# Kernel tuning notes

Hardware: AMD Instinct MI355X
Metric: run time of the kernel (lower is better)

Reference implementation:

```python
import jax, jax.numpy as jnp
import numpy as np

B, L, D = 1, 512, 128
DI = D // 2  # intermediate_dim = pair_dim // 2
EPS = 1e-5


def setup_inputs() -> dict:
    key = jax.random.key(0)
    ks = jax.random.split(key, 8)
    s = 0.02
    return {
        "pair": jax.random.normal(ks[0], (B, L, L, D), dtype=jnp.float32),
        "mask": jnp.ones((B, L, L), dtype=jnp.float32),
        "Wg1": jax.random.normal(ks[1], (D, DI), dtype=jnp.float32) * s,
        "bg1": jnp.zeros((DI,), dtype=jnp.float32),
        "Wg2": jax.random.normal(ks[2], (D, DI), dtype=jnp.float32) * s,
        "bg2": jnp.zeros((DI,), dtype=jnp.float32),
        "Wp": jax.random.normal(ks[3], (DI, D), dtype=jnp.float32) * s,
        "bp": jnp.zeros((D,), dtype=jnp.float32),
        "gamma": jnp.ones((D,), dtype=jnp.float32),
        "beta": jnp.zeros((D,), dtype=jnp.float32),
    }


def reference(pair, mask, Wg1, bg1, Wg2, bg2, Wp, bp, gamma, beta):
    # dual linear projections: [B,L,L,D] -> [B,L,L,DI]
    g1 = pair @ Wg1 + bg1
    g2 = pair @ Wg2 + bg2
    # outgoing triangle contraction: per-channel LxL matmul over k
    p = jnp.einsum("bikd,bkjd->bijd", g1, g2)  # [B,L,L,DI]
    p = p * mask[..., None]
    p = p @ Wp + bp  # [B,L,L,D]
    # dropout is identity in eval mode
    x = pair + p
    mu = jnp.mean(x, axis=-1, keepdims=True)
    var = jnp.var(x, axis=-1, keepdims=True)
    return (x - mu) * jax.lax.rsqrt(var + EPS) * gamma + beta
```

## Files before the change

kernel.cpp:

```cpp
#include <hip/hip_runtime.h>

#define L 512
#define LL (512*512)
#define D 128
#define DI 64

typedef unsigned short u16;
typedef short bf8 __attribute__((ext_vector_type(8)));
typedef float f4 __attribute__((ext_vector_type(4)));

union B8 { bf8 v; u16 u[8]; uint4 q; };

__device__ inline u16 f2bf(float f) {
  unsigned u = __builtin_bit_cast(unsigned, f);
  unsigned r = (u + 0x7FFFu + ((u >> 16) & 1u)) >> 16;
  return (u16)r;
}

__global__ __launch_bounds__(512)
void k1(const float* __restrict__ pair, const float* __restrict__ Wg1,
        const float* __restrict__ bg1, const float* __restrict__ Wg2,
        const float* __restrict__ bg2, u16* __restrict__ g1t, u16* __restrict__ g2t)
{
  __shared__ u16 WL[128*128];
  __shared__ u16 OL[64*256];
  const int tid = threadIdx.x;
  const int w = tid >> 6, lane = tid & 63;
  const int llo = lane & 15, lhi = lane >> 4;
  const int bx = blockIdx.x;
  const int i0 = (bx >> 5) << 4;
  const int c0 = (bx & 31) << 4;

  {
    const int n = tid >> 2;
    const int kb = (tid & 3) << 5;
    const float* src = (n < 64) ? (Wg1 + n) : (Wg2 + (n - 64));
    const int xr = (n & 7) << 3;
    for (int q = 0; q < 32; ++q) {
      int k = kb + q;
      WL[n*128 + (k ^ xr)] = f2bf(src[(size_t)k * 64]);
    }
  }
  __syncthreads();

  f4 acc[2][8];
  #pragma unroll
  for (int a = 0; a < 2; ++a)
    #pragma unroll
    for (int b = 0; b < 8; ++b) acc[a][b] = (f4){0.f,0.f,0.f,0.f};

  #pragma unroll
  for (int ks = 0; ks < 4; ++ks) {
    B8 bfr[8];
    const int kel = ks*32 + lhi*8;
    #pragma unroll
    for (int nf = 0; nf < 8; ++nf) {
      int n = nf*16 + llo;
      bfr[nf].q = *(const uint4*)&WL[n*128 + (kel ^ ((n & 7) << 3))];
    }
    #pragma unroll
    for (int mf = 0; mf < 2; ++mf) {
      int r = w*2 + mf;
      const float* ap = pair + (size_t)((i0 + r)*L + c0 + llo)*D + kel;
      float4 a0 = *(const float4*)ap;
      float4 a1 = *(const float4*)(ap + 4);
      B8 av;
      av.u[0]=f2bf(a0.x); av.u[1]=f2bf(a0.y); av.u[2]=f2bf(a0.z); av.u[3]=f2bf(a0.w);
      av.u[4]=f2bf(a1.x); av.u[5]=f2bf(a1.y); av.u[6]=f2bf(a1.z); av.u[7]=f2bf(a1.w);
      #pragma unroll
      for (int nf = 0; nf < 8; ++nf)
        acc[mf][nf] = __builtin_amdgcn_mfma_f32_16x16x32_bf16(av.v, bfr[nf].v, acc[mf][nf], 0, 0, 0);
    }
  }

  float bias[8];
  #pragma unroll
  for (int nf = 0; nf < 8; ++nf) {
    int n = nf*16 + llo;
    bias[nf] = (n < 64) ? bg1[n] : bg2[n - 64];
  }

  #pragma unroll
  for (int h = 0; h < 2; ++h) {
    __syncthreads();
    #pragma unroll
    for (int nf4 = 0; nf4 < 4; ++nf4) {
      const int nf = h*4 + nf4;
      const int chl = nf*16 + llo - h*64;
      const int xr = (chl & 7) << 2;
      #pragma unroll
      for (int mf = 0; mf < 2; ++mf) {
        const int r = w*2 + mf;
        const int cb = lhi*4;
        union { u16 h4[4]; uint2 d2; } vb;
        #pragma unroll
        for (int e = 0; e < 4; ++e) vb.h4[e] = f2bf(acc[mf][nf][e] + bias[nf]);
        if (h == 0) {
          int p = (r*16 + cb) ^ xr;
          *(uint2*)&OL[chl*256 + p] = vb.d2;
        } else {
          #pragma unroll
          for (int e = 0; e < 4; ++e)
            OL[chl*256 + (((cb + e)*16 + r) ^ xr)] = vb.h4[e];
        }
      }
    }
    __syncthreads();
    u16* dst0 = (h == 0) ? g1t : g2t;
    #pragma unroll
    for (int t2 = 0; t2 < 2; ++t2) {
      const int q = tid*2 + t2;
      const int chl = q >> 4;
      const int li = q & 15;
      const int xr = (chl & 7) << 2;
      union { u16 h4[16]; uint4 q4[2]; uint2 d2[4]; } tb;
      #pragma unroll
      for (int s = 0; s < 4; ++s) {
        int p = (li*16 + s*4) ^ xr;
        tb.d2[s] = *(const uint2*)&OL[chl*256 + p];
      }
      size_t off = (h == 0)
        ? ((size_t)chl*LL + (size_t)(i0 + li)*L + (size_t)c0)
        : ((size_t)chl*LL + (size_t)(c0 + li)*L + (size_t)i0);
      *(uint4*)(dst0 + off)     = tb.q4[0];
      *(uint4*)(dst0 + off + 8) = tb.q4[1];
    }
  }
}

__global__ __launch_bounds__(256)
void k2(const u16* __restrict__ g1t, const u16* __restrict__ g2t, u16* __restrict__ pt)
{
  __shared__ u16 SM[128*128];
  const int tid = threadIdx.x;
  const int lane = tid & 63, w = tid >> 6;
  const int llo = lane & 15, lhi = lane >> 4;
  const int bx = blockIdx.x;
  const int wg = ((bx & 7) << 7) | (bx >> 3);
  const int d  = wg >> 4;
  const int i0 = ((wg >> 2) & 3) << 7;
  const int j0 = (wg & 3) << 7;

  const u16* Ag = g1t + (size_t)d*LL;
  const u16* Yg = g2t + (size_t)d*LL;

  f4 acc[4][4];
  #pragma unroll
  for (int a = 0; a < 4; ++a)
    #pragma unroll
    for (int b = 0; b < 4; ++b) acc[a][b] = (f4){0.f,0.f,0.f,0.f};

  const int wr = (w >> 1) * 64, wc = (w & 1) * 64;

  const int srow = tid & 127;
  const u16* sg = (tid < 128) ? (Ag + (size_t)(i0 + srow)*L) : (Yg + (size_t)(j0 + srow)*L);
  u16* sl = (tid < 128) ? SM : (SM + 8192);
  const int sx = (srow & 7) << 3;

  for (int kt = 0; kt < 8; ++kt) {
    const int k0 = kt*64;
    #pragma unroll
    for (int q = 0; q < 8; ++q) {
      uint4 vv = *(const uint4*)(sg + k0 + q*8);
      *(uint4*)&sl[srow*64 + ((q*8) ^ sx)] = vv;
    }
    __syncthreads();
    #pragma unroll
    for (int ks = 0; ks < 2; ++ks) {
      B8 af[4], yf[4];
      const int kel = ks*32 + lhi*8;
      #pragma unroll
      for (int f = 0; f < 4; ++f) {
        int ra = wr + f*16 + llo;
        af[f].q = *(const uint4*)&SM[ra*64 + (kel ^ ((ra & 7) << 3))];
        int ry = wc + f*16 + llo;
        yf[f].q = *(const uint4*)&SM[8192 + ry*64 + (kel ^ ((ry & 7) << 3))];
      }
      #pragma unroll
      for (int mf = 0; mf < 4; ++mf)
        #pragma unroll
        for (int nf = 0; nf < 4; ++nf)
          acc[mf][nf] = __builtin_amdgcn_mfma_f32_16x16x32_bf16(af[mf].v, yf[nf].v, acc[mf][nf], 0, 0, 0);
    }
    __syncthreads();
  }

  #pragma unroll
  for (int mf = 0; mf < 4; ++mf) {
    #pragma unroll
    for (int nf = 0; nf < 4; ++nf) {
      const int jj = wc + nf*16 + llo;
      #pragma unroll
      for (int e = 0; e < 4; ++e) {
        const int ii = wr + mf*16 + lhi*4 + e;
        SM[ii*128 + (jj ^ ((ii & 7) << 3))] = f2bf(acc[mf][nf][e]);
      }
    }
  }
  __syncthreads();
  {
    const int ii = tid >> 1;
    const int half = (tid & 1) << 6;
    u16* dst = pt + (size_t)d*LL + (size_t)(i0 + ii)*L + j0 + half;
    const int xr = (ii & 7) << 3;
    #pragma unroll
    for (int q = 0; q < 8; ++q)
      *(uint4*)(dst + q*8) = *(const uint4*)&SM[ii*128 + ((half + q*8) ^ xr)];
  }
}

__global__ __launch_bounds__(256)
void k3(const u16* __restrict__ pt, const float* __restrict__ pair,
        const float* __restrict__ mask, const float* __restrict__ Wp,
        const float* __restrict__ bp, const float* __restrict__ gamma,
        const float* __restrict__ beta, float* __restrict__ out)
{
  __shared__ u16 PL[128*64];
  __shared__ u16 WT[128*64];
  __shared__ float MS[128];
  const int tid = threadIdx.x;
  const int lane = tid & 63, w = tid >> 6;
  const int llo = lane & 15, lhi = lane >> 4;
  const int bx = blockIdx.x;
  const int i  = bx >> 2;
  const int j0 = (bx & 3) << 7;

  {
    const int n = tid >> 1;
    const int dh = (tid & 1) << 5;
    const int xr = (n & 7) << 3;
    for (int q = 0; q < 32; ++q) {
      int dd = dh + q;
      WT[n*64 + (dd ^ xr)] = f2bf(Wp[(size_t)dd*128 + n]);
    }
  }
  if (tid < 128) MS[tid] = mask[(size_t)i*L + j0 + tid];
  {
    const int dd = tid >> 2;
    const u16* src = pt + (size_t)dd*LL + (size_t)i*L + j0;
    #pragma unroll
    for (int c = 0; c < 4; ++c) {
      const int jl = ((tid & 3)*4 + c) * 8;
      uint4 vv = *(const uint4*)(src + jl);
      const u16* pv = (const u16*)&vv;
      #pragma unroll
      for (int e = 0; e < 8; ++e) {
        int p = jl + e;
        PL[p*64 + (dd ^ ((p & 7) << 3))] = pv[e];
      }
    }
  }
  __syncthreads();

  f4 acc[2][8];
  #pragma unroll
  for (int a = 0; a < 2; ++a)
    #pragma unroll
    for (int b = 0; b < 8; ++b) acc[a][b] = (f4){0.f,0.f,0.f,0.f};

  #pragma unroll
  for (int ks = 0; ks < 2; ++ks) {
    const int kel = ks*32 + lhi*8;
    B8 bf[8];
    #pragma unroll
    for (int nf = 0; nf < 8; ++nf) {
      int n = nf*16 + llo;
      bf[nf].q = *(const uint4*)&WT[n*64 + (kel ^ ((n & 7) << 3))];
    }
    #pragma unroll
    for (int mf = 0; mf < 2; ++mf) {
      int p = w*32 + mf*16 + llo;
      B8 av;
      av.q = *(const uint4*)&PL[p*64 + (kel ^ ((p & 7) << 3))];
      #pragma unroll
      for (int nf = 0; nf < 8; ++nf)
        acc[mf][nf] = __builtin_amdgcn_mfma_f32_16x16x32_bf16(av.v, bf[nf].v, acc[mf][nf], 0, 0, 0);
    }
  }

  float bpv[8], gv[8], bv[8];
  #pragma unroll
  for (int nf = 0; nf < 8; ++nf) {
    int n = nf*16 + llo;
    bpv[nf] = bp[n]; gv[nf] = gamma[n]; bv[nf] = beta[n];
  }

  const size_t rowbase = (size_t)i*L + j0;
  #pragma unroll
  for (int mf = 0; mf < 2; ++mf) {
    #pragma unroll
    for (int e = 0; e < 4; ++e) {
      const int pl = w*32 + mf*16 + lhi*4 + e;
      const float mk = MS[pl];
      const float* prow = pair + (rowbase + pl)*D;
      float xv[8];
      float s1 = 0.f, s2 = 0.f;
      #pragma unroll
      for (int nf = 0; nf < 8; ++nf) {
        int n = nf*16 + llo;
        float x = prow[n] + mk*acc[mf][nf][e] + bpv[nf];
        xv[nf] = x; s1 += x; s2 += x*x;
      }
      #pragma unroll
      for (int m = 1; m < 16; m <<= 1) {
        s1 += __shfl_xor(s1, m);
        s2 += __shfl_xor(s2, m);
      }
      const float mu = s1 * (1.0f/128.0f);
      const float var = s2 * (1.0f/128.0f) - mu*mu;
      const float rs = rsqrtf(var + 1e-5f);
      float* orow = out + (rowbase + pl)*D;
      #pragma unroll
      for (int nf = 0; nf < 8; ++nf) {
        int n = nf*16 + llo;
        orow[n] = (xv[nf] - mu)*rs*gv[nf] + bv[nf];
      }
    }
  }
}

extern "C" void kernel_launch(void* const* d_in, const int* in_sizes, int n_in,
                              void* d_out, int out_size, void* d_ws, size_t ws_size,
                              hipStream_t stream) {
  (void)in_sizes; (void)n_in; (void)out_size; (void)ws_size;
  const float* pair = (const float*)d_in[0];
  const float* mask = (const float*)d_in[1];
  const float* Wg1  = (const float*)d_in[2];
  const float* bg1  = (const float*)d_in[3];
  const float* Wg2  = (const float*)d_in[4];
  const float* bg2  = (const float*)d_in[5];
  const float* Wp   = (const float*)d_in[6];
  const float* bp   = (const float*)d_in[7];
  const float* gamma= (const float*)d_in[8];
  const float* beta = (const float*)d_in[9];
  float* out = (float*)d_out;

  u16* g1t = (u16*)d_ws;
  u16* g2t = g1t + (size_t)DI*LL;
  u16* pt  = g2t + (size_t)DI*LL;

  hipLaunchKernelGGL(k1, dim3(1024), dim3(512), 0, stream,
                     pair, Wg1, bg1, Wg2, bg2, g1t, g2t);
  hipLaunchKernelGGL(k2, dim3(1024), dim3(256), 0, stream, g1t, g2t, pt);
  hipLaunchKernelGGL(k3, dim3(2048), dim3(256), 0, stream,
                     pt, pair, mask, Wp, bp, gamma, beta, out);
}
```

Baseline: 374.2 us.

## Pre-convert weights in a prep kernel, direct g1 stores, register-prefetch k2 tiles

```diff
diff --git a/kernel.cpp b/kernel.cpp
--- a/kernel.cpp
+++ b/kernel.cpp
@@ -17,13 +17,27 @@
   return (u16)r;
 }
 
+__global__ __launch_bounds__(256)
+void k0(const float* __restrict__ Wg1, const float* __restrict__ Wg2,
+        u16* __restrict__ WT)
+{
+  const int tid = threadIdx.x;
+  #pragma unroll
+  for (int it = 0; it < 4; ++it) {
+    const int E = blockIdx.x*1024 + it*256 + tid;
+    const int n = E >> 7, k = E & 127;
+    const float v = (n < 64) ? Wg1[(size_t)k*64 + n] : Wg2[(size_t)k*64 + (n - 64)];
+    WT[E] = f2bf(v);
+  }
+}
+
 __global__ __launch_bounds__(512)
-void k1(const float* __restrict__ pair, const float* __restrict__ Wg1,
-        const float* __restrict__ bg1, const float* __restrict__ Wg2,
-        const float* __restrict__ bg2, u16* __restrict__ g1t, u16* __restrict__ g2t)
+void k1(const float* __restrict__ pair, const u16* __restrict__ WT,
+        const float* __restrict__ bg1, const float* __restrict__ bg2,
+        u16* __restrict__ g1t, u16* __restrict__ g2t)
 {
   __shared__ u16 WL[128*128];
-  __shared__ u16 OL[64*256];
+  __shared__ u16 OL[32*256];
   const int tid = threadIdx.x;
   const int w = tid >> 6, lane = tid & 63;
   const int llo = lane & 15, lhi = lane >> 4;
@@ -31,15 +45,13 @@
   const int i0 = (bx >> 5) << 4;
   const int c0 = (bx & 31) << 4;
 
-  {
-    const int n = tid >> 2;
-    const int kb = (tid & 3) << 5;
-    const float* src = (n < 64) ? (Wg1 + n) : (Wg2 + (n - 64));
-    const int xr = (n & 7) << 3;
-    for (int q = 0; q < 32; ++q) {
-      int k = kb + q;
-      WL[n*128 + (k ^ xr)] = f2bf(src[(size_t)k * 64]);
-    }
+  #pragma unroll
+  for (int it = 0; it < 4; ++it) {
+    const int f = it*512 + tid;
+    const int E = f*8;
+    const int n = E >> 7, k = E & 127;
+    uint4 v = *(const uint4*)(WT + E);
+    *(uint4*)&WL[n*128 + (k ^ ((n & 7) << 3))] = v;
   }
   __syncthreads();
 
@@ -81,50 +93,48 @@
   }
 
   #pragma unroll
-  for (int h = 0; h < 2; ++h) {
-    __syncthreads();
-    #pragma unroll
-    for (int nf4 = 0; nf4 < 4; ++nf4) {
-      const int nf = h*4 + nf4;
-      const int chl = nf*16 + llo - h*64;
+  for (int nf = 0; nf < 4; ++nf) {
+    const int ch = nf*16 + llo;
+    #pragma unroll
+    for (int mf = 0; mf < 2; ++mf) {
+      const int r = w*2 + mf;
+      union { u16 h4[4]; uint2 d2; } vb;
+      #pragma unroll
+      for (int e = 0; e < 4; ++e) vb.h4[e] = f2bf(acc[mf][nf][e] + bias[nf]);
+      *(uint2*)(g1t + (size_t)ch*LL + (size_t)(i0 + r)*L + c0 + lhi*4) = vb.d2;
+    }
+  }
+
+  #pragma unroll
+  for (int sp = 0; sp < 2; ++sp) {
+    #pragma unroll
+    for (int nfl = 0; nfl < 2; ++nfl) {
+      const int nf = 4 + sp*2 + nfl;
+      const int chl = nfl*16 + llo;
       const int xr = (chl & 7) << 2;
       #pragma unroll
       for (int mf = 0; mf < 2; ++mf) {
         const int r = w*2 + mf;
         const int cb = lhi*4;
-        union { u16 h4[4]; uint2 d2; } vb;
         #pragma unroll
-        for (int e = 0; e < 4; ++e) vb.h4[e] = f2bf(acc[mf][nf][e] + bias[nf]);
-        if (h == 0) {
-          int p = (r*16 + cb) ^ xr;
-          *(uint2*)&OL[chl*256 + p] = vb.d2;
-        } else {
-          #pragma unroll
-          for (int e = 0; e < 4; ++e)
-            OL[chl*256 + (((cb + e)*16 + r) ^ xr)] = vb.h4[e];
-        }
+        for (int e = 0; e < 4; ++e)
+          OL[chl*256 + (((cb + e)*16 + r) ^ xr)] = f2bf(acc[mf][nf][e] + bias[nf]);
       }
     }
     __syncthreads();
-    u16* dst0 = (h == 0) ? g1t : g2t;
-    #pragma unroll
-    for (int t2 = 0; t2 < 2; ++t2) {
-      const int q = tid*2 + t2;
-      const int chl = q >> 4;
-      const int li = q & 15;
+    {
+      const int chl = tid >> 4;
+      const int li = tid & 15;
       const int xr = (chl & 7) << 2;
       union { u16 h4[16]; uint4 q4[2]; uint2 d2[4]; } tb;
       #pragma unroll
-      for (int s = 0; s < 4; ++s) {
-        int p = (li*16 + s*4) ^ xr;
-        tb.d2[s] = *(const uint2*)&OL[chl*256 + p];
-      }
-      size_t off = (h == 0)
-        ? ((size_t)chl*LL + (size_t)(i0 + li)*L + (size_t)c0)
-        : ((size_t)chl*LL + (size_t)(c0 + li)*L + (size_t)i0);
-      *(uint4*)(dst0 + off)     = tb.q4[0];
-      *(uint4*)(dst0 + off + 8) = tb.q4[1];
-    }
+      for (int s = 0; s < 4; ++s)
+        tb.d2[s] = *(const uint2*)&OL[chl*256 + ((li*16 + s*4) ^ xr)];
+      size_t off = (size_t)(sp*32 + chl)*LL + (size_t)(c0 + li)*L + (size_t)i0;
+      *(uint4*)(g2t + off)     = tb.q4[0];
+      *(uint4*)(g2t + off + 8) = tb.q4[1];
+    }
+    __syncthreads();
   }
 }
 
@@ -157,14 +167,19 @@
   u16* sl = (tid < 128) ? SM : (SM + 8192);
   const int sx = (srow & 7) << 3;
 
+  uint4 pf[8];
+  #pragma unroll
+  for (int q = 0; q < 8; ++q) pf[q] = *(const uint4*)(sg + q*8);
+  #pragma unroll
+  for (int q = 0; q < 8; ++q) *(uint4*)&sl[srow*64 + ((q*8) ^ sx)] = pf[q];
+  __syncthreads();
+
   for (int kt = 0; kt < 8; ++kt) {
-    const int k0 = kt*64;
-    #pragma unroll
-    for (int q = 0; q < 8; ++q) {
-      uint4 vv = *(const uint4*)(sg + k0 + q*8);
-      *(uint4*)&sl[srow*64 + ((q*8) ^ sx)] = vv;
-    }
-    __syncthreads();
+    if (kt < 7) {
+      const int k0 = (kt + 1) * 64;
+      #pragma unroll
+      for (int q = 0; q < 8; ++q) pf[q] = *(const uint4*)(sg + k0 + q*8);
+    }
     #pragma unroll
     for (int ks = 0; ks < 2; ++ks) {
       B8 af[4], yf[4];
@@ -181,6 +196,11 @@
         #pragma unroll
         for (int nf = 0; nf < 4; ++nf)
           acc[mf][nf] = __builtin_amdgcn_mfma_f32_16x16x32_bf16(af[mf].v, yf[nf].v, acc[mf][nf], 0, 0, 0);
+    }
+    __syncthreads();
+    if (kt < 7) {
+      #pragma unroll
+      for (int q = 0; q < 8; ++q) *(uint4*)&sl[srow*64 + ((q*8) ^ sx)] = pf[q];
     }
     __syncthreads();
   }
@@ -338,9 +358,11 @@
   u16* g1t = (u16*)d_ws;
   u16* g2t = g1t + (size_t)DI*LL;
   u16* pt  = g2t + (size_t)DI*LL;
-
+  u16* WTw = (u16*)d_out;
+
+  hipLaunchKernelGGL(k0, dim3(16), dim3(256), 0, stream, Wg1, Wg2, WTw);
   hipLaunchKernelGGL(k1, dim3(1024), dim3(512), 0, stream,
-                     pair, Wg1, bg1, Wg2, bg2, g1t, g2t);
+                     pair, WTw, bg1, bg2, g1t, g2t);
   hipLaunchKernelGGL(k2, dim3(1024), dim3(256), 0, stream, g1t, g2t, pt);
   hipLaunchKernelGGL(k3, dim3(2048), dim3(256), 0, stream,
                      pt, pair, mask, Wp, bp, gamma, beta, out);
```

Result: slower. 471.8 us (+26.1%).
